# Performance work log

Hardware: AMD Instinct MI355X
Metric: run time of the kernel (lower is better)

## Reference

```python
import jax, jax.numpy as jnp
import numpy as np

H = 16  # heads (query_heads == kv_heads in this config)
LN_EPS = 1e-5


def setup_inputs() -> dict:
    key = jax.random.key(0)
    ks = jax.random.split(key, 6)
    B, T, C = 4, 1024, 1024
    s = lambda fan_in: 1.0 / np.sqrt(fan_in)
    return {
        "x": jax.random.normal(ks[0], (B, T, C), jnp.float32),
        "c_attn_w": jax.random.normal(ks[1], (C, 3 * C), jnp.float32) * s(C),
        "c_attn_b": jnp.zeros((3 * C,), jnp.float32),
        "q_w": jax.random.normal(ks[2], (C, C), jnp.float32) * s(C),
        "q_b": jnp.zeros((C,), jnp.float32),
        "k_w": jax.random.normal(ks[3], (C, C), jnp.float32) * s(C),
        "k_b": jnp.zeros((C,), jnp.float32),
        "v_w": jax.random.normal(ks[4], (C, C), jnp.float32) * s(C),
        "v_b": jnp.zeros((C,), jnp.float32),
        "ln_g": jnp.ones((C,), jnp.float32),
        "ln_b": jnp.zeros((C,), jnp.float32),
        "out_w": jax.random.normal(ks[5], (C, C), jnp.float32) * s(C),
        "out_b": jnp.zeros((C,), jnp.float32),
    }


def reference(x, c_attn_w, c_attn_b, q_w, q_b, k_w, k_b, v_w, v_b,
              ln_g, ln_b, out_w, out_b):
    B, T, C = x.shape
    d = C // H
    # c_attn then split into query/key/value streams
    qkv = x @ c_attn_w + c_attn_b            # [B,T,3C]
    query, key_, value = jnp.split(qkv, 3, axis=-1)
    q = query @ q_w + q_b                     # [B,T,C]
    k = key_ @ k_w + k_b
    v = value @ v_w + v_b
    # split heads: b n (h d) -> b h n d
    q = q.reshape(B, T, H, d).transpose(0, 2, 1, 3)
    k = k.reshape(B, T, H, d).transpose(0, 2, 1, 3)
    v = v.reshape(B, T, H, d).transpose(0, 2, 1, 3)
    scale = d ** 0.5
    # NOTE: original code scales query by 1/scale AND the similarity by 1/scale
    # (net 1/d). Preserved faithfully.
    sim = jnp.einsum("bhnd,bhsd->bhns", q / scale, k)  # [B,H,T,T]
    causal = jnp.tril(jnp.ones((T, T), dtype=bool))
    sim = jnp.where(causal, sim, jnp.finfo(sim.dtype).min)
    attn = jax.nn.softmax(sim / scale, axis=-1)
    o = jnp.einsum("bhns,bhsd->bnhd", attn, v).reshape(B, T, C)
    # LayerNorm (eps=1e-5)
    mu = jnp.mean(o, axis=-1, keepdims=True)
    var = jnp.var(o, axis=-1, keepdims=True)
    o = (o - mu) * jax.lax.rsqrt(var + LN_EPS) * ln_g + ln_b
    return o @ out_w + out_b
```

## Files before the change

### kernel.cpp

```cpp
#include <hip/hip_runtime.h>
#include <hip/hip_bf16.h>
#include <stdint.h>

typedef __bf16 bf16_t;
typedef bf16_t bf16x4 __attribute__((ext_vector_type(4)));
typedef bf16_t bf16x8 __attribute__((ext_vector_type(8)));
typedef float  f32x4  __attribute__((ext_vector_type(4)));

#define B_   4
#define T_   1024
#define C_   1024
#define H_   16

__device__ __forceinline__ f32x4 mfma_bf16(bf16x8 a, bf16x8 b, f32x4 c) {
  return __builtin_amdgcn_mfma_f32_16x16x32_bf16(a, b, c, 0, 0, 0);
}

__device__ __forceinline__ void async16(const bf16_t* g, bf16_t* l) {
  __builtin_amdgcn_global_load_lds(
      (__attribute__((address_space(1))) void*)(uintptr_t)g,
      (__attribute__((address_space(3))) void*)l, 16, 0, 0);
}

__global__ __launch_bounds__(256) void convert_f32_bf16(
    const float* __restrict__ in, bf16_t* __restrict__ out, int n4)
{
  const int i = blockIdx.x * 256 + threadIdx.x;
  if (i >= n4) return;
  const float4 v = *(const float4*)(in + (size_t)i * 4);
  bf16x4 o;
  o[0] = (bf16_t)v.x; o[1] = (bf16_t)v.y; o[2] = (bf16_t)v.z; o[3] = (bf16_t)v.w;
  *(bf16x4*)(out + (size_t)i * 4) = o;
}

__global__ __launch_bounds__(256) void transpose4_f32_bf16(
    const float* __restrict__ a0, const float* __restrict__ a1,
    const float* __restrict__ a2, const float* __restrict__ a3,
    bf16_t* __restrict__ out)
{
  __shared__ bf16_t tile[32][33];
  const int z = blockIdx.z;
  const float* in = (z == 0) ? a0 : (z == 1) ? a1 : (z == 2) ? a2 : a3;
  bf16_t* o = out + ((size_t)z << 20);
  const int n0 = blockIdx.x * 32, k0 = blockIdx.y * 32;
  const int x = threadIdx.x & 31, y4 = (threadIdx.x >> 5) * 4;
#pragma unroll
  for (int i = 0; i < 4; ++i)
    tile[y4 + i][x] = (bf16_t)in[(size_t)(k0 + y4 + i) * 1024 + n0 + x];
  __syncthreads();
#pragma unroll
  for (int i = 0; i < 4; ++i)
    o[(size_t)(n0 + y4 + i) * 1024 + k0 + x] = tile[x][y4 + i];
}

__global__ __launch_bounds__(256) void transpose_v(
    const bf16_t* __restrict__ qkvb, bf16_t* __restrict__ vfrag)
{
  __shared__ bf16_t tile[64][66];
  const int bid = blockIdx.x;
  const int kb = bid & 15, bh = bid >> 4;
  const int b = bh >> 4, h = bh & 15;
  const int t = threadIdx.x;
  {
    const int key = t & 63, fc = (t >> 6) * 16;
    const bf16_t* src =
        qkvb + (size_t)(b * 1024 + kb * 64 + key) * 3072 + 2048 + h * 64 + fc;
    bf16x8 v0 = *(const bf16x8*)src;
    bf16x8 v1 = *(const bf16x8*)(src + 8);
#pragma unroll
    for (int j = 0; j < 8; ++j) {
      tile[fc + j][key]     = v0[j];
      tile[fc + 8 + j][key] = v1[j];
    }
  }
  __syncthreads();
#pragma unroll
  for (int ww = 0; ww < 2; ++ww) {
    const int g = t * 2 + ww;
    const int chunk = g >> 6;
    const int lane2 = g & 63;
    const int lr2 = lane2 & 15, lg2 = lane2 >> 4;
    const int kk = chunk >> 2, nf = chunk & 3;
    const int f = nf * 16 + lr2;
    const int key0 = kk * 32 + lg2 * 8;
    bf16x8 val;
#pragma unroll
    for (int j = 0; j < 8; ++j) val[j] = tile[f][key0 + j];
    *(bf16x8*)&vfrag[(((size_t)bh * 16 + kb) * 8 + chunk) * 512 + lane2 * 8] = val;
  }
}

__global__ __launch_bounds__(256) void bias_eff_kernel(
    const float* __restrict__ cb,
    const float* __restrict__ w0, const float* __restrict__ w1,
    const float* __restrict__ w2,
    const float* __restrict__ b0, const float* __restrict__ b1,
    const float* __restrict__ b2,
    float* __restrict__ out)
{
  __shared__ float part[4][64];
  const int j0 = blockIdx.x * 64;
  const int jl = threadIdx.x & 63, cq = threadIdx.x >> 6;
  const int j = j0 + jl;
  const int s = j >> 10, jj = j & 1023;
  const float* w  = (s == 0) ? w0 : (s == 1) ? w1 : w2;
  const float* sb = (s == 0) ? b0 : (s == 1) ? b1 : b2;
  float acc = 0.f;
  const int c0 = cq * 256;
#pragma unroll 8
  for (int c = c0; c < c0 + 256; ++c)
    acc += cb[s * 1024 + c] * w[(size_t)c * 1024 + jj];
  part[cq][jl] = acc;
  __syncthreads();
  if (cq == 0)
    out[j] = part[0][jl] + part[1][jl] + part[2][jl] + part[3][jl] + sb[jj];
}

template <typename OT>
__global__ __launch_bounds__(256) void gemm_bt_bias(
    const bf16_t* __restrict__ A, int lda,
    const bf16_t* __restrict__ Bt, int ldb,
    const float* __restrict__ bias,
    OT* __restrict__ C, int ldc,
    int K, int nTilesN, int blocksPerMat,
    int strideA, int strideB, int strideC, int xcdSwz)
{
  __shared__ __align__(16) bf16_t As[2][128 * 32];
  __shared__ __align__(16) bf16_t Bs[2][128 * 32];
  int raw = blockIdx.x;
  if (xcdSwz) {
    const int cpx = gridDim.x >> 3;
    raw = (raw & 7) * cpx + (raw >> 3);
  }
  const int s   = raw / blocksPerMat;
  const int bid = raw % blocksPerMat;
  A  += (size_t)s * strideA;
  Bt += (size_t)s * strideB;
  C  += (size_t)s * strideC;
  const int mt = bid / nTilesN, nt = bid % nTilesN;
  const int m0 = mt * 128, n0 = nt * 128;
  const int tid = threadIdx.x;
  const int lane = tid & 63;
  const int lr = lane & 15, lg = lane >> 4;
  const int wid = tid >> 6;
  const int wr = wid >> 1, wc = wid & 1;
  const int sLg = lg ^ ((lr >> 1) & 3);

  f32x4 acc[4][4];
#pragma unroll
  for (int m = 0; m < 4; ++m)
#pragma unroll
    for (int n = 0; n < 4; ++n) acc[m][n] = (f32x4){0.f, 0.f, 0.f, 0.f};

  const int nk = K >> 5;
  int cur = 0;
#pragma unroll
  for (int p = 0; p < 2; ++p) {
    const int c = p * 256 + tid;
    const int row = c >> 2;
    const int col = (((c & 3) ^ ((c >> 3) & 3)) << 3);
    async16(A + (size_t)(m0 + row) * lda + col, &As[0][c * 8]);
    async16(Bt + (size_t)(n0 + row) * ldb + col, &Bs[0][c * 8]);
  }
  __syncthreads();

  for (int t = 0; t < nk; ++t) {
    if (t + 1 < nk) {
      const int k0 = (t + 1) << 5;
#pragma unroll
      for (int p = 0; p < 2; ++p) {
        const int c = p * 256 + tid;
        const int row = c >> 2;
        const int col = (((c & 3) ^ ((c >> 3) & 3)) << 3);
        async16(A + (size_t)(m0 + row) * lda + k0 + col, &As[cur ^ 1][c * 8]);
        async16(Bt + (size_t)(n0 + row) * ldb + k0 + col, &Bs[cur ^ 1][c * 8]);
      }
    }
    bf16x8 af[4], bfr[4];
#pragma unroll
    for (int m = 0; m < 4; ++m)
      af[m] = *(const bf16x8*)&As[cur][(wr * 64 + m * 16 + lr) * 32 + sLg * 8];
#pragma unroll
    for (int n = 0; n < 4; ++n)
      bfr[n] = *(const bf16x8*)&Bs[cur][(wc * 64 + n * 16 + lr) * 32 + sLg * 8];
#pragma unroll
    for (int m = 0; m < 4; ++m)
#pragma unroll
      for (int n = 0; n < 4; ++n)
        acc[m][n] = mfma_bf16(af[m], bfr[n], acc[m][n]);
    __syncthreads();
    cur ^= 1;
  }

#pragma unroll
  for (int n = 0; n < 4; ++n) {
    const int col = n0 + wc * 64 + n * 16 + lr;
    const float bv = bias ? bias[col] : 0.0f;
#pragma unroll
    for (int m = 0; m < 4; ++m) {
      const int row = m0 + wr * 64 + m * 16 + lg * 4;
#pragma unroll
      for (int r = 0; r < 4; ++r)
        C[(size_t)(row + r) * ldc + col] = (OT)(acc[m][n][r] + bv);
    }
  }
}

__global__ __launch_bounds__(256) void attn_kernel(
    const bf16_t* __restrict__ qkv, const bf16_t* __restrict__ vfrag,
    bf16_t* __restrict__ o)
{
  __shared__ __align__(16) bf16_t Ks[2][8][512];
  __shared__ __align__(16) bf16_t Vs[2][8][512];
  __shared__ __align__(16) bf16_t Ps[4][16][72];
  const int LD = 3072;
  const bf16_t* q = qkv;
  const bf16_t* k = qkv + 1024;

  const int raw = blockIdx.x;
  const int xcd = raw & 7, idx = raw >> 3;
  const int bh   = (idx >> 3) * 8 + xcd;
  const int slot = idx & 7;
  const int b = bh >> 4, h = bh & 15;

  const int tid = threadIdx.x;
  const int lane = tid & 63;
  const int lr = lane & 15, lg = lane >> 4;
  const int w = tid >> 6;

  const bf16_t* kbase = k + (size_t)(b * T_) * LD + h * 64;
  const bf16_t* vfbase = vfrag + (size_t)bh * 16 * 8 * 512;

  auto stage = [&](int bf, int it) {
    const int kv0 = it << 6;
#pragma unroll
    for (int cc = 0; cc < 4; ++cc) {
      const int c = w * 4 + cc;
      if (c < 8) {
        const int kg = c >> 1, kk = c & 1;
        async16(kbase + (size_t)(kv0 + kg * 16 + lr) * LD + kk * 32 + lg * 8,
                &Ks[bf][c][lane * 8]);
      } else {
        const int cv = c - 8;
        async16(vfbase + ((size_t)it * 8 + cv) * 512 + lane * 8,
                &Vs[bf][cv][lane * 8]);
      }
    }
  };

#pragma unroll
  for (int pass = 0; pass < 2; ++pass) {
    const int band = pass ? (15 - slot) : slot;
    const int myq = band * 64 + w * 16 + lr;
    const int nIter = band + 1;

    bf16x8 qf[2];
    {
      const size_t qr = (size_t)(b * T_ + myq) * LD + h * 64;
      qf[0] = *(const bf16x8*)&q[qr + lg * 8];
      qf[1] = *(const bf16x8*)&q[qr + 32 + lg * 8];
    }

    float mi = -3.0e38f, li = 0.0f;
    f32x4 acc[4];
#pragma unroll
    for (int nf = 0; nf < 4; ++nf) acc[nf] = (f32x4){0.f, 0.f, 0.f, 0.f};

    stage(0, 0);
    __syncthreads();

    for (int it = 0; it < nIter; ++it) {
      const int bf = it & 1;
      if (it + 1 < nIter) stage(bf ^ 1, it + 1);
      const int kv0 = it << 6;

      f32x4 sfr[4];
      __builtin_amdgcn_s_setprio(1);
#pragma unroll
      for (int kg = 0; kg < 4; ++kg) {
        bf16x8 kf0 = *(const bf16x8*)&Ks[bf][kg * 2 + 0][lane * 8];
        bf16x8 kf1 = *(const bf16x8*)&Ks[bf][kg * 2 + 1][lane * 8];
        f32x4 z = (f32x4){0.f, 0.f, 0.f, 0.f};
        z = mfma_bf16(kf0, qf[0], z);
        z = mfma_bf16(kf1, qf[1], z);
        sfr[kg] = z;
      }
      __builtin_amdgcn_s_setprio(0);

      float sv[4][4];
      float pm[4];
#pragma unroll
      for (int kg = 0; kg < 4; ++kg) {
        const int keyb = kv0 + kg * 16 + lg * 4;
        pm[kg] = -3.0e38f;
#pragma unroll
        for (int r = 0; r < 4; ++r) {
          float xx = sfr[kg][r] * 0.015625f;
          if (keyb + r > myq) xx = -3.0e38f;
          sv[kg][r] = xx;
          pm[kg] = fmaxf(pm[kg], xx);
        }
      }
      float pmax = fmaxf(fmaxf(pm[0], pm[1]), fmaxf(pm[2], pm[3]));
      pmax = fmaxf(pmax, __shfl_xor(pmax, 16));
      pmax = fmaxf(pmax, __shfl_xor(pmax, 32));
      const float mnew = fmaxf(mi, pmax);
      const float fr = __expf(mi - mnew);
      mi = mnew;
      float ps[4];
#pragma unroll
      for (int kg = 0; kg < 4; ++kg) {
        float p0 = __expf(sv[kg][0] - mi);
        float p1 = __expf(sv[kg][1] - mi);
        float p2 = __expf(sv[kg][2] - mi);
        float p3 = __expf(sv[kg][3] - mi);
        sv[kg][0] = p0; sv[kg][1] = p1; sv[kg][2] = p2; sv[kg][3] = p3;
        ps[kg] = (p0 + p1) + (p2 + p3);
      }
      float psum = (ps[0] + ps[1]) + (ps[2] + ps[3]);
      psum += __shfl_xor(psum, 16);
      psum += __shfl_xor(psum, 32);
      li = li * fr + psum;
#pragma unroll
      for (int nf = 0; nf < 4; ++nf)
#pragma unroll
        for (int r = 0; r < 4; ++r) acc[nf][r] *= fr;

#pragma unroll
      for (int kg = 0; kg < 4; ++kg) {
        bf16x4 p4;
#pragma unroll
        for (int r = 0; r < 4; ++r) p4[r] = (bf16_t)sv[kg][r];
        *(bf16x4*)&Ps[w][lr][kg * 16 + lg * 4] = p4;
      }

      __builtin_amdgcn_s_setprio(1);
#pragma unroll
      for (int kk = 0; kk < 2; ++kk) {
        bf16x8 pf = *(const bf16x8*)&Ps[w][lr][kk * 32 + lg * 8];
#pragma unroll
        for (int nf = 0; nf < 4; ++nf) {
          bf16x8 vf = *(const bf16x8*)&Vs[bf][kk * 4 + nf][lane * 8];
          acc[nf] = mfma_bf16(vf, pf, acc[nf]);
        }
      }
      __builtin_amdgcn_s_setprio(0);

      __syncthreads();
    }

    const float inv = 1.0f / li;
#pragma unroll
    for (int nf = 0; nf < 4; ++nf) {
      bf16x4 o4;
#pragma unroll
      for (int r = 0; r < 4; ++r) o4[r] = (bf16_t)(acc[nf][r] * inv);
      *(bf16x4*)&o[(size_t)(b * T_ + myq) * C_ + h * 64 + nf * 16 + lg * 4] = o4;
    }
  }
}

__global__ __launch_bounds__(256) void ln_kernel(
    const bf16_t* __restrict__ in,
    const float* __restrict__ g,
    const float* __restrict__ be,
    bf16_t* __restrict__ out)
{
  const int row = blockIdx.x * 4 + (threadIdx.x >> 6);
  const int lane = threadIdx.x & 63;
  const bf16_t* p = in + (size_t)row * C_ + lane * 16;
  bf16x8 a0 = *(const bf16x8*)p;
  bf16x8 a1 = *(const bf16x8*)(p + 8);
  float xs[16];
#pragma unroll
  for (int j = 0; j < 8; ++j) { xs[j] = (float)a0[j]; xs[8 + j] = (float)a1[j]; }
  float sum = 0.f, sq = 0.f;
#pragma unroll
  for (int j = 0; j < 16; ++j) { sum += xs[j]; sq += xs[j] * xs[j]; }
#pragma unroll
  for (int dd = 1; dd < 64; dd <<= 1) {
    sum += __shfl_xor(sum, dd);
    sq  += __shfl_xor(sq, dd);
  }
  const float mean = sum * (1.0f / 1024.0f);
  const float var  = sq * (1.0f / 1024.0f) - mean * mean;
  const float rstd = rsqrtf(var + 1e-5f);
  float gv[16], bv[16];
#pragma unroll
  for (int j = 0; j < 4; ++j) {
    *(float4*)&gv[j * 4] = *(const float4*)(g  + lane * 16 + j * 4);
    *(float4*)&bv[j * 4] = *(const float4*)(be + lane * 16 + j * 4);
  }
  bf16x8 o0, o1;
#pragma unroll
  for (int j = 0; j < 8; ++j) {
    o0[j] = (bf16_t)((xs[j] - mean) * rstd * gv[j] + bv[j]);
    o1[j] = (bf16_t)((xs[8 + j] - mean) * rstd * gv[8 + j] + bv[8 + j]);
  }
  bf16_t* op = out + (size_t)row * C_ + lane * 16;
  *(bf16x8*)op = o0;
  *(bf16x8*)(op + 8) = o1;
}

extern "C" void kernel_launch(void* const* d_in, const int* in_sizes, int n_in,
                              void* d_out, int out_size, void* d_ws, size_t ws_size,
                              hipStream_t stream)
{
  const float* x        = (const float*)d_in[0];
  const float* c_attn_w = (const float*)d_in[1];
  const float* c_attn_b = (const float*)d_in[2];
  const float* q_w      = (const float*)d_in[3];
  const float* q_b      = (const float*)d_in[4];
  const float* k_w      = (const float*)d_in[5];
  const float* k_b      = (const float*)d_in[6];
  const float* v_w      = (const float*)d_in[7];
  const float* v_b      = (const float*)d_in[8];
  const float* ln_g     = (const float*)d_in[9];
  const float* ln_b     = (const float*)d_in[10];
  const float* out_w    = (const float*)d_in[11];
  const float* out_b    = (const float*)d_in[12];

  char* ws = (char*)d_ws;
  bf16_t* qkvb      = (bf16_t*)(ws + 0);
  bf16_t* xb        = (bf16_t*)(ws + 25165824);
  bf16_t* lnb       = (bf16_t*)(ws + 25165824);
  bf16_t* WsT4      = (bf16_t*)(ws + 33554432);
  bf16_t* c_attn_wb = (bf16_t*)(ws + 41943040);
  bf16_t* Wt_eff    = (bf16_t*)(ws + 48234496);
  float*  bias_eff  = (float*)(ws + 54525952);
  bf16_t* vfrag     = (bf16_t*)(ws + 54538240);

  convert_f32_bf16<<<dim3(4096), 256, 0, stream>>>(x, xb, 1048576);
  convert_f32_bf16<<<dim3(3072), 256, 0, stream>>>(c_attn_w, c_attn_wb, 786432);

  transpose4_f32_bf16<<<dim3(32, 32, 4), 256, 0, stream>>>(
      q_w, k_w, v_w, out_w, WsT4);

  gemm_bt_bias<bf16_t><<<dim3(192), 256, 0, stream>>>(
      WsT4, 1024, c_attn_wb, 3072, nullptr, Wt_eff, 1024,
      1024, 8, 64, 1 << 20, 1024, 1 << 20, 0);

  bias_eff_kernel<<<dim3(48), 256, 0, stream>>>(
      c_attn_b, q_w, k_w, v_w, q_b, k_b, v_b, bias_eff);

  gemm_bt_bias<bf16_t><<<dim3(768), 256, 0, stream>>>(
      xb, 1024, Wt_eff, 1024, bias_eff, qkvb, 3072, 1024, 24, 768, 0, 0, 0, 1);

  transpose_v<<<dim3(1024), 256, 0, stream>>>(qkvb, vfrag);

  attn_kernel<<<dim3(512), 256, 0, stream>>>(qkvb, vfrag, (bf16_t*)d_out);

  ln_kernel<<<dim3(1024), 256, 0, stream>>>((const bf16_t*)d_out, ln_g, ln_b, lnb);

  gemm_bt_bias<float><<<dim3(256), 256, 0, stream>>>(
      lnb, 1024, WsT4 + (size_t)3 * (1 << 20), 1024, out_b,
      (float*)d_out, 1024, 1024, 8, 256, 0, 0, 0, 1);
}
```

Before: 160.1 us.

## Add 256x256-tile 4-stage pipelined GEMM for the fused QKV projection

Introduces a new GEMM kernel with 256x256 output tiles, 512 threads (8 waves), and a 4-deep async global-to-LDS pipeline with explicit vmcnt waits, XCD-aware block remapping and setprio around MFMA. It replaces the 128x128-tile generic GEMM for the x @ Wt_eff QKV projection. The goal is higher arithmetic intensity per LDS load and better latency hiding. In exchange it uses 128KB of LDS and only 192 blocks, which risks low occupancy and poor wave balance across CUs.

```diff
diff --git a/kernel.cpp b/kernel.cpp
--- a/kernel.cpp
+++ b/kernel.cpp
@@ -206,6 +206,100 @@
   }
 }
 
+__global__ __launch_bounds__(512, 2) void gemm256(
+    const bf16_t* __restrict__ A, int lda,
+    const bf16_t* __restrict__ Bt, int ldb,
+    const float* __restrict__ bias,
+    bf16_t* __restrict__ C, int ldc,
+    int K, int nTilesN)
+{
+  __shared__ __align__(16) bf16_t As[4][256 * 32];
+  __shared__ __align__(16) bf16_t Bs[4][256 * 32];
+  int raw = blockIdx.x;
+  {
+    const int cpx = gridDim.x >> 3;
+    raw = (raw & 7) * cpx + (raw >> 3);
+  }
+  const int mt = raw / nTilesN, nt = raw % nTilesN;
+  const int m0 = mt * 256, n0 = nt * 256;
+  const int tid = threadIdx.x;
+  const int lane = tid & 63;
+  const int lr = lane & 15, lg = lane >> 4;
+  const int wid = tid >> 6;
+  const int wm = wid >> 2, wn = wid & 3;
+
+  f32x4 acc[8][4];
+#pragma unroll
+  for (int m = 0; m < 8; ++m)
+#pragma unroll
+    for (int n = 0; n < 4; ++n) acc[m][n] = (f32x4){0.f, 0.f, 0.f, 0.f};
+
+  const int nk = K >> 5;
+
+  auto stage = [&](int buf, int t) {
+    const int k0 = t << 5;
+#pragma unroll
+    for (int p = 0; p < 2; ++p) {
+      const int c = p * 512 + tid;
+      const int row = c >> 2, col = (c & 3) << 3;
+      async16(A + (size_t)(m0 + row) * lda + k0 + col, &As[buf][c * 8]);
+      async16(Bt + (size_t)(n0 + row) * ldb + k0 + col, &Bs[buf][c * 8]);
+    }
+  };
+
+  stage(0, 0);
+  stage(1, 1);
+  stage(2, 2);
+  asm volatile("s_waitcnt vmcnt(8)" ::: "memory");
+  __builtin_amdgcn_sched_barrier(0);
+  __builtin_amdgcn_s_barrier();
+  __builtin_amdgcn_sched_barrier(0);
+
+  for (int t = 0; t < nk; ++t) {
+    const int buf = t & 3;
+    if (t + 3 < nk) stage((t + 3) & 3, t + 3);
+
+    bf16x8 af[8], bfr[4];
+#pragma unroll
+    for (int m = 0; m < 8; ++m)
+      af[m] = *(const bf16x8*)&As[buf][(wm * 128 + m * 16 + lr) * 32 + lg * 8];
+#pragma unroll
+    for (int n = 0; n < 4; ++n)
+      bfr[n] = *(const bf16x8*)&Bs[buf][(wn * 64 + n * 16 + lr) * 32 + lg * 8];
+
+    if (t + 3 < nk)
+      asm volatile("s_waitcnt lgkmcnt(0) vmcnt(8)" ::: "memory");
+    else if (t + 3 == nk)
+      asm volatile("s_waitcnt lgkmcnt(0) vmcnt(4)" ::: "memory");
+    else
+      asm volatile("s_waitcnt lgkmcnt(0) vmcnt(0)" ::: "memory");
+    __builtin_amdgcn_sched_barrier(0);
+    __builtin_amdgcn_s_barrier();
+    __builtin_amdgcn_sched_barrier(0);
+
+    __builtin_amdgcn_s_setprio(1);
+#pragma unroll
+    for (int m = 0; m < 8; ++m)
+#pragma unroll
+      for (int n = 0; n < 4; ++n)
+        acc[m][n] = mfma_bf16(af[m], bfr[n], acc[m][n]);
+    __builtin_amdgcn_s_setprio(0);
+  }
+
+#pragma unroll
+  for (int n = 0; n < 4; ++n) {
+    const int col = n0 + wn * 64 + n * 16 + lr;
+    const float bv = bias ? bias[col] : 0.0f;
+#pragma unroll
+    for (int m = 0; m < 8; ++m) {
+      const int row = m0 + wm * 128 + m * 16 + lg * 4;
+#pragma unroll
+      for (int r = 0; r < 4; ++r)
+        C[(size_t)(row + r) * ldc + col] = (bf16_t)(acc[m][n][r] + bv);
+    }
+  }
+}
+
 __global__ __launch_bounds__(256) void attn_kernel(
     const bf16_t* __restrict__ qkv, const bf16_t* __restrict__ vfrag,
     bf16_t* __restrict__ o)
@@ -443,8 +537,8 @@
   bias_eff_kernel<<<dim3(48), 256, 0, stream>>>(
       c_attn_b, q_w, k_w, v_w, q_b, k_b, v_b, bias_eff);
 
-  gemm_bt_bias<bf16_t><<<dim3(768), 256, 0, stream>>>(
-      xb, 1024, Wt_eff, 1024, bias_eff, qkvb, 3072, 1024, 24, 768, 0, 0, 0, 1);
+  gemm256<<<dim3(192), 512, 0, stream>>>(
+      xb, 1024, Wt_eff, 1024, bias_eff, qkvb, 3072, 1024, 12);
 
   transpose_v<<<dim3(1024), 256, 0, stream>>>(qkvb, vfrag);
 
```

Measured after the change: 170.3 us. +6.4%, slower.

## Triple-buffer GEMM LDS staging with explicit vmcnt waits and one barrier per step

Applied to the files above, without the earlier changes.

Converts the bf16 GEMM's double-buffered async global-to-LDS pipeline into a three-stage pipeline that prefetches two K-tiles ahead. Hand-placed s_waitcnt vmcnt/lgkmcnt counts and a single s_barrier per iteration replace the trailing __syncthreads. The MFMA block runs at raised wave priority. This is meant to hide global load latency and cut sync stalls, at the cost of 50% more LDS per block (48KB), which may lower occupancy. It also depends on exact counter values matching the number of issued async loads.

```diff
diff --git a/kernel.cpp b/kernel.cpp
--- a/kernel.cpp
+++ b/kernel.cpp
@@ -125,8 +125,8 @@
     int K, int nTilesN, int blocksPerMat,
     int strideA, int strideB, int strideC, int xcdSwz)
 {
-  __shared__ __align__(16) bf16_t As[2][128 * 32];
-  __shared__ __align__(16) bf16_t Bs[2][128 * 32];
+  __shared__ __align__(16) bf16_t As[3][128 * 32];
+  __shared__ __align__(16) bf16_t Bs[3][128 * 32];
   int raw = blockIdx.x;
   if (xcdSwz) {
     const int cpx = gridDim.x >> 3;
@@ -153,43 +153,53 @@
     for (int n = 0; n < 4; ++n) acc[m][n] = (f32x4){0.f, 0.f, 0.f, 0.f};
 
   const int nk = K >> 5;
-  int cur = 0;
-#pragma unroll
-  for (int p = 0; p < 2; ++p) {
-    const int c = p * 256 + tid;
-    const int row = c >> 2;
-    const int col = (((c & 3) ^ ((c >> 3) & 3)) << 3);
-    async16(A + (size_t)(m0 + row) * lda + col, &As[0][c * 8]);
-    async16(Bt + (size_t)(n0 + row) * ldb + col, &Bs[0][c * 8]);
-  }
-  __syncthreads();
+
+  auto stage = [&](int buf, int t) {
+    const int k0 = t << 5;
+#pragma unroll
+    for (int p = 0; p < 2; ++p) {
+      const int c = p * 256 + tid;
+      const int row = c >> 2;
+      const int col = (((c & 3) ^ ((c >> 3) & 3)) << 3);
+      async16(A + (size_t)(m0 + row) * lda + k0 + col, &As[buf][c * 8]);
+      async16(Bt + (size_t)(n0 + row) * ldb + k0 + col, &Bs[buf][c * 8]);
+    }
+  };
+
+  stage(0, 0);
+  stage(1, 1);
+  asm volatile("s_waitcnt vmcnt(4)" ::: "memory");
+  __builtin_amdgcn_sched_barrier(0);
+  __builtin_amdgcn_s_barrier();
+  __builtin_amdgcn_sched_barrier(0);
 
   for (int t = 0; t < nk; ++t) {
-    if (t + 1 < nk) {
-      const int k0 = (t + 1) << 5;
-#pragma unroll
-      for (int p = 0; p < 2; ++p) {
-        const int c = p * 256 + tid;
-        const int row = c >> 2;
-        const int col = (((c & 3) ^ ((c >> 3) & 3)) << 3);
-        async16(A + (size_t)(m0 + row) * lda + k0 + col, &As[cur ^ 1][c * 8]);
-        async16(Bt + (size_t)(n0 + row) * ldb + k0 + col, &Bs[cur ^ 1][c * 8]);
-      }
-    }
+    const int buf = t % 3;
+    if (t + 2 < nk) stage((t + 2) % 3, t + 2);
+
     bf16x8 af[4], bfr[4];
 #pragma unroll
     for (int m = 0; m < 4; ++m)
-      af[m] = *(const bf16x8*)&As[cur][(wr * 64 + m * 16 + lr) * 32 + sLg * 8];
+      af[m] = *(const bf16x8*)&As[buf][(wr * 64 + m * 16 + lr) * 32 + sLg * 8];
 #pragma unroll
     for (int n = 0; n < 4; ++n)
-      bfr[n] = *(const bf16x8*)&Bs[cur][(wc * 64 + n * 16 + lr) * 32 + sLg * 8];
+      bfr[n] = *(const bf16x8*)&Bs[buf][(wc * 64 + n * 16 + lr) * 32 + sLg * 8];
+
+    if (t + 2 < nk)
+      asm volatile("s_waitcnt lgkmcnt(0) vmcnt(4)" ::: "memory");
+    else
+      asm volatile("s_waitcnt lgkmcnt(0) vmcnt(0)" ::: "memory");
+    __builtin_amdgcn_sched_barrier(0);
+    __builtin_amdgcn_s_barrier();
+    __builtin_amdgcn_sched_barrier(0);
+
+    __builtin_amdgcn_s_setprio(1);
 #pragma unroll
     for (int m = 0; m < 4; ++m)
 #pragma unroll
       for (int n = 0; n < 4; ++n)
         acc[m][n] = mfma_bf16(af[m], bfr[n], acc[m][n]);
-    __syncthreads();
-    cur ^= 1;
+    __builtin_amdgcn_s_setprio(0);
   }
 
 #pragma unroll
```

Measured after the change: 160.1 us. Within noise of the previous version (+0.0%).
